# Optimization experiments

Hardware: AMD Instinct MI355X
Metric: run time of the kernel (lower is better)

Reference implementation:

```python
import jax, jax.numpy as jnp
import numpy as np
from jax import lax

RHO = 1.0
LAMDA = 0.1
ADMM_ITERS = 10


def setup_inputs() -> dict:
    key = jax.random.key(0)
    k1, k2, k3, k4 = jax.random.split(key, 4)
    B, M, A, MULT = 2048, 512, 2048, 3
    S = A * MULT
    y = jax.random.normal(k1, (B, M), dtype=jnp.float32)
    x = jax.random.normal(k2, (B, A), dtype=jnp.float32)
    # measurement matrix buffer: randn(m, ambient)/sqrt(m)
    a = jax.random.normal(k3, (M, A), dtype=jnp.float32) / np.sqrt(M)
    # phi: kaiming_normal_ on (ambient*mult, ambient): std = sqrt(2/fan_in)
    phi = jax.random.normal(k4, (S, A), dtype=jnp.float32) * np.sqrt(2.0 / A)
    return {"y": y, "x": x, "a": a, "phi": phi}


def _shrink(v, thresh):
    return jnp.sign(v) * jnp.maximum(jnp.zeros_like(v), jnp.abs(v) - thresh)


def reference(y, x, a, phi):
    B = y.shape[0]
    x = x.reshape(B, -1)
    y = y.reshape(B, -1)
    min_x = jnp.min(x)
    max_x = jnp.max(x)
    S = phi.shape[0]
    u = jnp.zeros((B, S), dtype=y.dtype)
    z = jnp.zeros((B, S), dtype=y.dtype)

    # multiplier(rho): m = a^T a + rho * phi^T phi, LU-factor, invert L and U.
    m = a.T @ a + RHO * (phi.T @ phi)
    _, L, U = jax.scipy.linalg.lu(m)
    # NOTE: original uses einsum('aa,ba->ba', Linv, v) which contracts the
    # repeated index -> uses only diag(Linv) elementwise. Replicate exactly.
    dL = jnp.diagonal(jnp.linalg.inv(L))  # (A,) -- unit-lower -> ones
    dU = jnp.diagonal(jnp.linalg.inv(U))  # (A,)

    # x0 = einsum('am,bm->ba', a.T, y) = y @ a  -> (B, A)
    x0 = y @ a
    rho_phi = RHO * phi  # (S, A)

    def step(carry, _):
        u, z, _xh = carry
        # einsum('as,bs->ba', rho*phi.T, z-u) = (z-u) @ (rho*phi)
        x_L = dL * (x0 + (z - u) @ rho_phi)            # (B, A)
        x_hat = dU * x_L                                # (B, A)
        fxu = x_hat @ phi.T + u                         # (B, S)
        z_new = _shrink(fxu, LAMDA / RHO)
        u_new = u + fxu - z_new
        return (u_new, z_new, x_hat), None

    xh0 = jnp.zeros((B, x.shape[1]), dtype=y.dtype)
    (u, z, x_hat), _ = lax.scan(step, (u, z, xh0), None, length=ADMM_ITERS)
    return jnp.clip(x_hat, min_x, max_x)
```

## Files before the change

### kernel.cpp

```cpp
#include <hip/hip_runtime.h>

#define B_N 2048
#define M_N 512
#define A_N 2048
#define S_N 6144
#define SHRINK_T 0.1f
#define ADMM_ITERS 10

#define SPLIT_SCALE 512.0f
#define INV_SPLIT (1.0f / 512.0f)

typedef _Float16 v8h __attribute__((ext_vector_type(8)));
typedef _Float16 v4h __attribute__((ext_vector_type(4)));
typedef float v4f __attribute__((ext_vector_type(4)));

#define AS1 __attribute__((address_space(1)))
#define AS3 __attribute__((address_space(3)))

__device__ __forceinline__ float shrinkf(float v) {
  return copysignf(fmaxf(fabsf(v) - SHRINK_T, 0.f), v);
}

__device__ __forceinline__ void dma16(const _Float16* g, int ld, int r0, int k0,
                                      int slot, _Float16* region) {
  int m = slot >> 2;
  int k8 = (slot & 3) ^ ((m >> 1) & 3);
  const _Float16* gp = g + (size_t)(r0 + m) * ld + k0 + (k8 << 3);
  __builtin_amdgcn_global_load_lds((const AS1 void*)gp,
                                   (AS3 void*)(region + (size_t)(slot & ~63) * 8), 16, 0, 0);
}

template <int EPI>
__global__ __launch_bounds__(256, 2) void mgemm(
    const _Float16* __restrict__ Ah0, const _Float16* __restrict__ Al0, int ldA0, int K0,
    const _Float16* __restrict__ Bh0, const _Float16* __restrict__ Bl0, int ldB0,
    const _Float16* __restrict__ Ah1, const _Float16* __restrict__ Al1, int ldA1, int K1,
    const _Float16* __restrict__ Bh1, const _Float16* __restrict__ Bl1, int ldB1,
    float* __restrict__ C, int ldC, const float* __restrict__ dU,
    _Float16* __restrict__ Oh, _Float16* __restrict__ Ol, float* __restrict__ U) {
  __shared__ _Float16 lds[16384];
  const int tid = threadIdx.x;
  const int i0 = blockIdx.y * 128, j0 = blockIdx.x * 128;
  const int lane = tid & 63, w = tid >> 6, wm = w >> 1, wn = w & 1;
  const int fb = (lane & 15) * 32 + (((lane >> 4) ^ ((lane >> 1) & 3)) << 3);

  v4f acc1[4][4], acc2[4][4];
  const v4f z4 = {0.f, 0.f, 0.f, 0.f};
#pragma unroll
  for (int tm = 0; tm < 4; ++tm)
#pragma unroll
    for (int tn = 0; tn < 4; ++tn) { acc1[tm][tn] = z4; acc2[tm][tn] = z4; }

  auto phase = [&](const _Float16* Ah, const _Float16* Al, int ldA,
                   const _Float16* Bh, const _Float16* Bl, int ldB, int K) {
    for (int k0 = 0; k0 < K; k0 += 32) {
      __syncthreads();
      dma16(Ah, ldA, i0, k0, tid,        lds);
      dma16(Ah, ldA, i0, k0, 256 + tid,  lds);
      dma16(Al, ldA, i0, k0, tid,        lds + 4096);
      dma16(Al, ldA, i0, k0, 256 + tid,  lds + 4096);
      dma16(Bh, ldB, j0, k0, tid,        lds + 8192);
      dma16(Bh, ldB, j0, k0, 256 + tid,  lds + 8192);
      dma16(Bl, ldB, j0, k0, tid,        lds + 12288);
      dma16(Bl, ldB, j0, k0, 256 + tid,  lds + 12288);
      __syncthreads();
      v8h ah[4], al[4], bh[4], bl[4];
#pragma unroll
      for (int tm = 0; tm < 4; ++tm) {
        int off = (wm * 64 + tm * 16) * 32 + fb;
        ah[tm] = *(const v8h*)(lds + off);
        al[tm] = *(const v8h*)(lds + 4096 + off);
      }
#pragma unroll
      for (int tn = 0; tn < 4; ++tn) {
        int off = (wn * 64 + tn * 16) * 32 + fb;
        bh[tn] = *(const v8h*)(lds + 8192 + off);
        bl[tn] = *(const v8h*)(lds + 12288 + off);
      }
#pragma unroll
      for (int tm = 0; tm < 4; ++tm)
#pragma unroll
        for (int tn = 0; tn < 4; ++tn) {
          acc1[tm][tn] = __builtin_amdgcn_mfma_f32_16x16x32_f16(ah[tm], bh[tn], acc1[tm][tn], 0, 0, 0);
          v4f c2 = acc2[tm][tn];
          c2 = __builtin_amdgcn_mfma_f32_16x16x32_f16(ah[tm], bl[tn], c2, 0, 0, 0);
          c2 = __builtin_amdgcn_mfma_f32_16x16x32_f16(al[tm], bh[tn], c2, 0, 0, 0);
          acc2[tm][tn] = c2;
        }
    }
  };
  phase(Ah0, Al0, ldA0, Bh0, Bl0, ldB0, K0);
  if (K1 > 0) phase(Ah1, Al1, ldA1, Bh1, Bl1, ldB1, K1);

  const int q = lane >> 4, lr = lane & 15;
#pragma unroll
  for (int tm = 0; tm < 4; ++tm)
#pragma unroll
    for (int tn = 0; tn < 4; ++tn) {
      int row0 = i0 + wm * 64 + tm * 16 + q * 4;
      int col = j0 + wn * 64 + tn * 16 + lr;
      if constexpr (EPI == 0) {
#pragma unroll
        for (int r = 0; r < 4; ++r) {
          size_t o = (size_t)(row0 + r) * ldC + col;
          C[o] = acc1[tm][tn][r] + acc2[tm][tn][r] * INV_SPLIT;
        }
      } else if constexpr (EPI == 1) {
        float du = dU[col];
#pragma unroll
        for (int r = 0; r < 4; ++r) {
          size_t o = (size_t)(row0 + r) * ldC + col;
          float v = (acc1[tm][tn][r] + acc2[tm][tn][r] * INV_SPLIT) * du;
          C[o] = v;
          _Float16 h = (_Float16)v;
          Oh[o] = h;
          Ol[o] = (_Float16)((v - (float)h) * SPLIT_SCALE);
        }
      } else {
#pragma unroll
        for (int r = 0; r < 4; ++r) {
          size_t o = (size_t)(row0 + r) * ldC + col;
          float uo = U[o];
          float fx = acc1[tm][tn][r] + acc2[tm][tn][r] * INV_SPLIT + uo;
          float zn = shrinkf(fx);
          float un = uo + fx - zn;
          U[o] = un;
          float zu = zn - un;
          _Float16 h = (_Float16)zu;
          Oh[o] = h;
          Ol[o] = (_Float16)((zu - (float)h) * SPLIT_SCALE);
        }
      }
    }
}

__global__ __launch_bounds__(256) void split_kernel(const float* __restrict__ s,
                                                    _Float16* __restrict__ h,
                                                    _Float16* __restrict__ l, int n4) {
  for (int i = blockIdx.x * 256 + threadIdx.x; i < n4; i += gridDim.x * 256) {
    float4 v = ((const float4*)s)[i];
    v4h hh, ll;
    hh.x = (_Float16)v.x; ll.x = (_Float16)((v.x - (float)hh.x) * SPLIT_SCALE);
    hh.y = (_Float16)v.y; ll.y = (_Float16)((v.y - (float)hh.y) * SPLIT_SCALE);
    hh.z = (_Float16)v.z; ll.z = (_Float16)((v.z - (float)hh.z) * SPLIT_SCALE);
    hh.w = (_Float16)v.w; ll.w = (_Float16)((v.w - (float)hh.w) * SPLIT_SCALE);
    ((v4h*)h)[i] = hh;
    ((v4h*)l)[i] = ll;
  }
}

__global__ __launch_bounds__(256) void tsplit_kernel(const float* __restrict__ src, int R, int C,
                                                     _Float16* __restrict__ h,
                                                     _Float16* __restrict__ l) {
  __shared__ float t[32][33];
  int br = blockIdx.y * 32, bc = blockIdx.x * 32;
  int r = threadIdx.x >> 3, c4 = (threadIdx.x & 7) * 4;
  float4 v = *(const float4*)(src + (size_t)(br + r) * C + bc + c4);
  t[r][c4 + 0] = v.x; t[r][c4 + 1] = v.y; t[r][c4 + 2] = v.z; t[r][c4 + 3] = v.w;
  __syncthreads();
  int a = threadIdx.x >> 3, r4 = (threadIdx.x & 7) * 4;
  float x0 = t[r4 + 0][a], x1 = t[r4 + 1][a], x2 = t[r4 + 2][a], x3 = t[r4 + 3][a];
  v4h hh, ll;
  hh.x = (_Float16)x0; ll.x = (_Float16)((x0 - (float)hh.x) * SPLIT_SCALE);
  hh.y = (_Float16)x1; ll.y = (_Float16)((x1 - (float)hh.y) * SPLIT_SCALE);
  hh.z = (_Float16)x2; ll.z = (_Float16)((x2 - (float)hh.z) * SPLIT_SCALE);
  hh.w = (_Float16)x3; ll.w = (_Float16)((x3 - (float)hh.w) * SPLIT_SCALE);
  size_t o = (size_t)(bc + a) * R + br + r4;
  *(v4h*)(h + o) = hh;
  *(v4h*)(l + o) = ll;
}

__global__ __launch_bounds__(256) void chol64_kernel(float* __restrict__ mm,
                                                     float* __restrict__ dU, int kb) {
  __shared__ float Ad[64][65];
  int tid = threadIdx.x;
  for (int e = tid; e < 64 * 64; e += 256) {
    int r = e >> 6, c = e & 63;
    Ad[r][c] = mm[(size_t)(kb + r) * A_N + kb + c];
  }
  __syncthreads();
  for (int j = 0; j < 64; ++j) {
    if (tid == 0) Ad[j][j] = sqrtf(Ad[j][j]);
    __syncthreads();
    if (tid > j && tid < 64) Ad[tid][j] /= Ad[j][j];
    __syncthreads();
    int i = j + 1 + (tid >> 2);
    int q = tid & 3;
    if (i < 64) {
      float lij = Ad[i][j];
      for (int t = j + 1 + q; t <= i; t += 4)
        Ad[i][t] = fmaf(-lij, Ad[t][j], Ad[i][t]);
    }
    __syncthreads();
  }
  if (tid < 64) {
    float d = Ad[tid][tid];
    dU[kb + tid] = 1.0f / (d * d);
  }
  for (int e = tid; e < 64 * 64; e += 256) {
    int r = e >> 6, c = e & 63;
    if (c <= r) mm[(size_t)(kb + r) * A_N + kb + c] = Ad[r][c];
  }
}

__global__ __launch_bounds__(256) void trsm64_kernel(float* __restrict__ mm, int kb) {
  __shared__ float Ls[64][65];
  int tid = threadIdx.x;
  for (int e = tid; e < 64 * 64; e += 256) {
    int r = e >> 6, c = e & 63;
    Ls[r][c] = mm[(size_t)(kb + r) * A_N + kb + c];
  }
  __syncthreads();
  int row = kb + 64 + blockIdx.x * 256 + tid;
  if (row >= A_N) return;
  float v[64];
  float* gr = mm + (size_t)row * A_N + kb;
#pragma unroll
  for (int qq = 0; qq < 16; ++qq) {
    float4 t = *(const float4*)(gr + qq * 4);
    v[qq * 4 + 0] = t.x; v[qq * 4 + 1] = t.y;
    v[qq * 4 + 2] = t.z; v[qq * 4 + 3] = t.w;
  }
#pragma unroll
  for (int j = 0; j < 64; ++j) {
    float s = v[j];
#pragma unroll
    for (int t = 0; t < j; ++t) s = fmaf(-v[t], Ls[j][t], s);
    v[j] = s / Ls[j][j];
  }
#pragma unroll
  for (int qq = 0; qq < 16; ++qq)
    *(float4*)(gr + qq * 4) =
        make_float4(v[qq * 4 + 0], v[qq * 4 + 1], v[qq * 4 + 2], v[qq * 4 + 3]);
}

__global__ __launch_bounds__(256) void syrk64_kernel(float* __restrict__ mm, int kb) {
  __shared__ float As[16 * 64];
  __shared__ float Bs[16 * 64];
  int tid = threadIdx.x, tx = tid & 15, ty = tid >> 4;
  int base = kb + 64;
  int i0 = base + blockIdx.y * 64;
  int j0 = base + blockIdx.x * 64;
  float acc[4][4] = {{0.f}};
  for (int k0 = 0; k0 < 64; k0 += 16) {
    __syncthreads();
    {
      int ii = tid >> 2, k4 = (tid & 3) * 4;
      float4 vv = *(const float4*)(mm + (size_t)(i0 + ii) * A_N + kb + k0 + k4);
      As[(k4 + 0) * 64 + ii] = vv.x; As[(k4 + 1) * 64 + ii] = vv.y;
      As[(k4 + 2) * 64 + ii] = vv.z; As[(k4 + 3) * 64 + ii] = vv.w;
      float4 ww = *(const float4*)(mm + (size_t)(j0 + ii) * A_N + kb + k0 + k4);
      Bs[(k4 + 0) * 64 + ii] = ww.x; Bs[(k4 + 1) * 64 + ii] = ww.y;
      Bs[(k4 + 2) * 64 + ii] = ww.z; Bs[(k4 + 3) * 64 + ii] = ww.w;
    }
    __syncthreads();
#pragma unroll
    for (int k = 0; k < 16; ++k) {
      float4 a0 = *(const float4*)(As + k * 64 + ty * 4);
      float4 b0 = *(const float4*)(Bs + k * 64 + tx * 4);
      float av[4] = {a0.x, a0.y, a0.z, a0.w};
      float bv[4] = {b0.x, b0.y, b0.z, b0.w};
#pragma unroll
      for (int i = 0; i < 4; ++i)
#pragma unroll
        for (int j = 0; j < 4; ++j) acc[i][j] = fmaf(av[i], bv[j], acc[i][j]);
    }
  }
#pragma unroll
  for (int i = 0; i < 4; ++i) {
    float* p = mm + (size_t)(i0 + ty * 4 + i) * A_N + j0 + tx * 4;
    float4 c = *(const float4*)p;
    c.x -= acc[i][0]; c.y -= acc[i][1]; c.z -= acc[i][2]; c.w -= acc[i][3];
    *(float4*)p = c;
  }
}

__device__ __forceinline__ unsigned fkey(float v) {
  unsigned b = __float_as_uint(v);
  return (b & 0x80000000u) ? ~b : (b | 0x80000000u);
}
__device__ __forceinline__ float key2f(unsigned k) {
  unsigned b = (k & 0x80000000u) ? (k & 0x7FFFFFFFu) : ~k;
  return __uint_as_float(b);
}

__global__ void minmax_init(unsigned* keys) {
  keys[0] = 0xFFFFFFFFu;
  keys[1] = 0u;
}

__global__ __launch_bounds__(256) void minmax_kernel(const float* __restrict__ x,
                                                     unsigned* __restrict__ keys, int n4) {
  unsigned mn = 0xFFFFFFFFu, mx = 0u;
  for (int i = blockIdx.x * 256 + threadIdx.x; i < n4; i += gridDim.x * 256) {
    float4 v = ((const float4*)x)[i];
    unsigned k0 = fkey(v.x), k1 = fkey(v.y), k2 = fkey(v.z), k3 = fkey(v.w);
    mn = min(mn, min(min(k0, k1), min(k2, k3)));
    mx = max(mx, max(max(k0, k1), max(k2, k3)));
  }
  for (int o = 32; o > 0; o >>= 1) {
    mn = min(mn, (unsigned)__shfl_down((int)mn, o));
    mx = max(mx, (unsigned)__shfl_down((int)mx, o));
  }
  if ((threadIdx.x & 63) == 0) {
    atomicMin(&keys[0], mn);
    atomicMax(&keys[1], mx);
  }
}

__global__ __launch_bounds__(256) void clip_kernel(const float* __restrict__ xh,
                                                   const unsigned* __restrict__ keys,
                                                   float* __restrict__ out, int n4) {
  float mn = key2f(keys[0]);
  float mx = key2f(keys[1]);
  for (int i = blockIdx.x * 256 + threadIdx.x; i < n4; i += gridDim.x * 256) {
    float4 v = ((const float4*)xh)[i];
    v.x = fminf(fmaxf(v.x, mn), mx);
    v.y = fminf(fmaxf(v.y, mn), mx);
    v.z = fminf(fmaxf(v.z, mn), mx);
    v.w = fminf(fmaxf(v.w, mn), mx);
    ((float4*)out)[i] = v;
  }
}

extern "C" void kernel_launch(void* const* d_in, const int* in_sizes, int n_in,
                              void* d_out, int out_size, void* d_ws, size_t ws_size,
                              hipStream_t stream) {
  const float* y   = (const float*)d_in[0];
  const float* x   = (const float*)d_in[1];
  const float* a   = (const float*)d_in[2];
  const float* phi = (const float*)d_in[3];
  float* out = (float*)d_out;

  char* ws = (char*)d_ws;
  size_t off = 0;
  auto alloc = [&](size_t bytes) -> void* {
    void* p = ws + off;
    off = (off + bytes + 255) & ~(size_t)255;
    return p;
  };
  float* mm = (float*)alloc(sizeof(float) * (size_t)A_N * A_N);
  float* u  = (float*)alloc(sizeof(float) * (size_t)B_N * S_N);
  float* dU = (float*)alloc(sizeof(float) * A_N);
  unsigned* keys = (unsigned*)alloc(sizeof(unsigned) * 2);
  _Float16* phi_h  = (_Float16*)alloc(2 * (size_t)S_N * A_N);
  _Float16* phi_l  = (_Float16*)alloc(2 * (size_t)S_N * A_N);
  _Float16* phiT_h = (_Float16*)alloc(2 * (size_t)A_N * S_N);
  _Float16* phiT_l = (_Float16*)alloc(2 * (size_t)A_N * S_N);
  _Float16* aT_h   = (_Float16*)alloc(2 * (size_t)A_N * M_N);
  _Float16* aT_l   = (_Float16*)alloc(2 * (size_t)A_N * M_N);
  _Float16* y_h    = (_Float16*)alloc(2 * (size_t)B_N * M_N);
  _Float16* y_l    = (_Float16*)alloc(2 * (size_t)B_N * M_N);
  _Float16* zu_h   = (_Float16*)alloc(2 * (size_t)B_N * S_N);
  _Float16* zu_l   = (_Float16*)alloc(2 * (size_t)B_N * S_N);
  _Float16* xh_h   = (_Float16*)alloc(2 * (size_t)B_N * A_N);
  _Float16* xh_l   = (_Float16*)alloc(2 * (size_t)B_N * A_N);
  float* xh32 = mm;

  minmax_init<<<1, 1, 0, stream>>>(keys);
  minmax_kernel<<<1024, 256, 0, stream>>>(x, keys, (B_N * A_N) / 4);

  split_kernel<<<2048, 256, 0, stream>>>(phi, phi_h, phi_l, (S_N * A_N) / 4);
  split_kernel<<<512, 256, 0, stream>>>(y, y_h, y_l, (B_N * M_N) / 4);
  tsplit_kernel<<<dim3(A_N / 32, S_N / 32), 256, 0, stream>>>(phi, S_N, A_N, phiT_h, phiT_l);
  tsplit_kernel<<<dim3(A_N / 32, M_N / 32), 256, 0, stream>>>(a, M_N, A_N, aT_h, aT_l);

  mgemm<0><<<dim3(A_N / 128, A_N / 128), 256, 0, stream>>>(
      aT_h, aT_l, M_N, M_N, aT_h, aT_l, M_N,
      phiT_h, phiT_l, S_N, S_N, phiT_h, phiT_l, S_N,
      mm, A_N, nullptr, nullptr, nullptr, nullptr);

  for (int kb = 0; kb < A_N; kb += 64) {
    chol64_kernel<<<1, 256, 0, stream>>>(mm, dU, kb);
    int rows = A_N - kb - 64;
    if (rows > 0) {
      trsm64_kernel<<<(rows + 255) / 256, 256, 0, stream>>>(mm, kb);
      syrk64_kernel<<<dim3(rows / 64, rows / 64), 256, 0, stream>>>(mm, kb);
    }
  }

  hipMemsetAsync(u, 0, sizeof(float) * (size_t)B_N * S_N, stream);
  hipMemsetAsync(zu_h, 0, 2 * (size_t)B_N * S_N, stream);
  hipMemsetAsync(zu_l, 0, 2 * (size_t)B_N * S_N, stream);

  for (int it = 0; it < ADMM_ITERS; ++it) {
    mgemm<1><<<dim3(A_N / 128, B_N / 128), 256, 0, stream>>>(
        zu_h, zu_l, S_N, S_N, phiT_h, phiT_l, S_N,
        y_h, y_l, M_N, M_N, aT_h, aT_l, M_N,
        xh32, A_N, dU, xh_h, xh_l, nullptr);
    if (it < ADMM_ITERS - 1) {
      mgemm<2><<<dim3(S_N / 128, B_N / 128), 256, 0, stream>>>(
          xh_h, xh_l, A_N, A_N, phi_h, phi_l, A_N,
          nullptr, nullptr, 0, 0, nullptr, nullptr, 0,
          nullptr, S_N, nullptr, zu_h, zu_l, u);
    }
  }

  clip_kernel<<<1024, 256, 0, stream>>>(xh32, keys, out, (B_N * A_N) / 4);
}
```

Baseline: 7.555 ms.

## Double-buffer LDS tiles in split-fp16 GEMM to overlap loads with MFMA

Doubles the shared-memory tile buffer. The two K phases are merged into one unified step loop that prefetches the next K-slice via global_load_lds into the alternate buffer while the current slice feeds the MFMAs. This cuts barriers from two per step to one and hides global-load latency behind compute. LDS per block doubles to 64KB, which still allows two blocks per CU but may pressure occupancy.

```diff
diff --git a/kernel.cpp b/kernel.cpp
--- a/kernel.cpp
+++ b/kernel.cpp
@@ -38,7 +38,7 @@
     const _Float16* __restrict__ Bh1, const _Float16* __restrict__ Bl1, int ldB1,
     float* __restrict__ C, int ldC, const float* __restrict__ dU,
     _Float16* __restrict__ Oh, _Float16* __restrict__ Ol, float* __restrict__ U) {
-  __shared__ _Float16 lds[16384];
+  __shared__ _Float16 lds[2 * 16384];
   const int tid = threadIdx.x;
   const int i0 = blockIdx.y * 128, j0 = blockIdx.x * 128;
   const int lane = tid & 63, w = tid >> 6, wm = w >> 1, wn = w & 1;
@@ -51,46 +51,57 @@
 #pragma unroll
     for (int tn = 0; tn < 4; ++tn) { acc1[tm][tn] = z4; acc2[tm][tn] = z4; }
 
-  auto phase = [&](const _Float16* Ah, const _Float16* Al, int ldA,
-                   const _Float16* Bh, const _Float16* Bl, int ldB, int K) {
-    for (int k0 = 0; k0 < K; k0 += 32) {
-      __syncthreads();
-      dma16(Ah, ldA, i0, k0, tid,        lds);
-      dma16(Ah, ldA, i0, k0, 256 + tid,  lds);
-      dma16(Al, ldA, i0, k0, tid,        lds + 4096);
-      dma16(Al, ldA, i0, k0, 256 + tid,  lds + 4096);
-      dma16(Bh, ldB, j0, k0, tid,        lds + 8192);
-      dma16(Bh, ldB, j0, k0, 256 + tid,  lds + 8192);
-      dma16(Bl, ldB, j0, k0, tid,        lds + 12288);
-      dma16(Bl, ldB, j0, k0, 256 + tid,  lds + 12288);
-      __syncthreads();
-      v8h ah[4], al[4], bh[4], bl[4];
-#pragma unroll
-      for (int tm = 0; tm < 4; ++tm) {
-        int off = (wm * 64 + tm * 16) * 32 + fb;
-        ah[tm] = *(const v8h*)(lds + off);
-        al[tm] = *(const v8h*)(lds + 4096 + off);
+  const int steps0 = K0 >> 5, steps1 = K1 >> 5, total = steps0 + steps1;
+
+  auto issue = [&](int s, _Float16* buf) {
+    const _Float16 *Ah, *Al, *Bh, *Bl;
+    int ldA, ldB, k0;
+    if (s < steps0) {
+      Ah = Ah0; Al = Al0; Bh = Bh0; Bl = Bl0; ldA = ldA0; ldB = ldB0; k0 = s << 5;
+    } else {
+      Ah = Ah1; Al = Al1; Bh = Bh1; Bl = Bl1; ldA = ldA1; ldB = ldB1; k0 = (s - steps0) << 5;
+    }
+    dma16(Ah, ldA, i0, k0, tid,       buf);
+    dma16(Ah, ldA, i0, k0, 256 + tid, buf);
+    dma16(Al, ldA, i0, k0, tid,       buf + 4096);
+    dma16(Al, ldA, i0, k0, 256 + tid, buf + 4096);
+    dma16(Bh, ldB, j0, k0, tid,       buf + 8192);
+    dma16(Bh, ldB, j0, k0, 256 + tid, buf + 8192);
+    dma16(Bl, ldB, j0, k0, tid,       buf + 12288);
+    dma16(Bl, ldB, j0, k0, 256 + tid, buf + 12288);
+  };
+
+  issue(0, lds);
+  int cur = 0;
+  for (int s = 0; s < total; ++s) {
+    __syncthreads();
+    if (s + 1 < total) issue(s + 1, lds + (cur ^ 1) * 16384);
+    const _Float16* L = lds + cur * 16384;
+    v8h ah[4], al[4], bh[4], bl[4];
+#pragma unroll
+    for (int tm = 0; tm < 4; ++tm) {
+      int off = (wm * 64 + tm * 16) * 32 + fb;
+      ah[tm] = *(const v8h*)(L + off);
+      al[tm] = *(const v8h*)(L + 4096 + off);
+    }
+#pragma unroll
+    for (int tn = 0; tn < 4; ++tn) {
+      int off = (wn * 64 + tn * 16) * 32 + fb;
+      bh[tn] = *(const v8h*)(L + 8192 + off);
+      bl[tn] = *(const v8h*)(L + 12288 + off);
+    }
+#pragma unroll
+    for (int tm = 0; tm < 4; ++tm)
+#pragma unroll
+      for (int tn = 0; tn < 4; ++tn) {
+        acc1[tm][tn] = __builtin_amdgcn_mfma_f32_16x16x32_f16(ah[tm], bh[tn], acc1[tm][tn], 0, 0, 0);
+        v4f c2 = acc2[tm][tn];
+        c2 = __builtin_amdgcn_mfma_f32_16x16x32_f16(ah[tm], bl[tn], c2, 0, 0, 0);
+        c2 = __builtin_amdgcn_mfma_f32_16x16x32_f16(al[tm], bh[tn], c2, 0, 0, 0);
+        acc2[tm][tn] = c2;
       }
-#pragma unroll
-      for (int tn = 0; tn < 4; ++tn) {
-        int off = (wn * 64 + tn * 16) * 32 + fb;
-        bh[tn] = *(const v8h*)(lds + 8192 + off);
-        bl[tn] = *(const v8h*)(lds + 12288 + off);
-      }
-#pragma unroll
-      for (int tm = 0; tm < 4; ++tm)
-#pragma unroll
-        for (int tn = 0; tn < 4; ++tn) {
-          acc1[tm][tn] = __builtin_amdgcn_mfma_f32_16x16x32_f16(ah[tm], bh[tn], acc1[tm][tn], 0, 0, 0);
-          v4f c2 = acc2[tm][tn];
-          c2 = __builtin_amdgcn_mfma_f32_16x16x32_f16(ah[tm], bl[tn], c2, 0, 0, 0);
-          c2 = __builtin_amdgcn_mfma_f32_16x16x32_f16(al[tm], bh[tn], c2, 0, 0, 0);
-          acc2[tm][tn] = c2;
-        }
-    }
-  };
-  phase(Ah0, Al0, ldA0, Bh0, Bl0, ldB0, K0);
-  if (K1 > 0) phase(Ah1, Al1, ldA1, Bh1, Bl1, ldB1, K1);
+    cur ^= 1;
+  }
 
   const int q = lane >> 4, lr = lane & 15;
 #pragma unroll
```

New measurement: 6.892 ms. 1.1x faster.
